# Kernel optimization log

Hardware: AMD Instinct MI355X
Metric: run time of the kernel (lower is better)

Reference implementation:

```python
import jax, jax.numpy as jnp
import numpy as np

D_HIDDEN = 1024
N_HEAD = 16
D_HEAD = D_HIDDEN // N_HEAD  # 64
B, F = 4, 2048


def setup_inputs() -> dict:
    key = jax.random.key(0)
    ks = jax.random.split(key, 10)
    std = 0.02
    inp = {
        "q": jax.random.normal(ks[0], (B, F, D_HIDDEN), jnp.float32),
        "k": jax.random.normal(ks[1], (B, F, D_HIDDEN), jnp.float32),
        "v": jax.random.normal(ks[2], (B, F, D_HIDDEN), jnp.float32),
        # additive mask: 1 = masked position (scaled by -1e9 inside); all-zero = no masking
        "attention_mask": jnp.zeros((B, F, F), jnp.float32),
        # Dense layer params (Keras Dense: y = x @ W + b)
        "qw_w": jax.random.truncated_normal(ks[3], -2, 2, (D_HIDDEN, D_HIDDEN), jnp.float32) * std,
        "qw_b": jnp.zeros((D_HIDDEN,), jnp.float32),
        "kw_w": jax.random.truncated_normal(ks[4], -2, 2, (D_HIDDEN, D_HIDDEN), jnp.float32) * std,
        "kw_b": jnp.zeros((D_HIDDEN,), jnp.float32),
        "vw_w": jax.random.truncated_normal(ks[5], -2, 2, (D_HIDDEN, D_HIDDEN), jnp.float32) * std,
        "vw_b": jnp.zeros((D_HIDDEN,), jnp.float32),
        # output projection kernel (n_head, d_head, d_hidden)
        "out_kernel": jax.random.truncated_normal(ks[6], -2, 2, (N_HEAD, D_HEAD, D_HIDDEN), jnp.float32) * std,
    }
    return inp


def reference(q, k, v, attention_mask, qw_w, qw_b, kw_w, kw_b, vw_w, vw_b, out_kernel):
    b, f, _ = q.shape
    # linear projections
    qh = q @ qw_w + qw_b
    kh = k @ kw_w + kw_b
    vh = v @ vw_w + vw_b
    # split heads: [B, F, H, D] -> [B, H, F, D]
    def split(x):
        return x.reshape(b, -1, N_HEAD, D_HEAD).transpose(0, 2, 1, 3)
    qh, kh, vh = split(qh), split(kh), split(vh)
    # scaled dot-product attention with additive mask (1 -> -1e9)
    scores = jnp.einsum('BNFD,BNfD->BNFf', qh, kh) / jnp.sqrt(jnp.asarray(D_HEAD, qh.dtype))
    scores = scores + attention_mask[:, None, :, :] * jnp.asarray(-1e9, scores.dtype)
    probs = jax.nn.softmax(scores, axis=-1)
    out = jnp.einsum('BNFf,BNfD->BNFD', probs, vh)
    out = out.transpose(0, 2, 1, 3)  # BNFD -> BFND
    return jnp.einsum('BFND,NDM->BFM', out, out_kernel)
```

## Files before the change

kernel.cpp:

```cpp
#include <hip/hip_runtime.h>


typedef unsigned short u16;
typedef __attribute__((ext_vector_type(8))) short short8;
typedef __attribute__((ext_vector_type(4))) float f32x4;
typedef __attribute__((ext_vector_type(16))) float f32x16;

#define SC2 0.18033688011112042f
#define MSC -1.4426950408889634e9f
#define THR 8.0f

__device__ __forceinline__ u16 f2bf(float x) {
  unsigned int u = __float_as_uint(x);
  u += 0x7FFFu + ((u >> 16) & 1u);
  return (u16)(u >> 16);
}

__device__ __forceinline__ void gload16(const void* g, void* l) {
  __builtin_amdgcn_global_load_lds(
      (const __attribute__((address_space(1))) void*)g,
      (__attribute__((address_space(3))) void*)l, 16, 0, 0);
}

__device__ __forceinline__ uint4 pack8(const u16* t) {
  uint4 o;
  o.x = (unsigned)t[0] | ((unsigned)t[1] << 16);
  o.y = (unsigned)t[2] | ((unsigned)t[3] << 16);
  o.z = (unsigned)t[4] | ((unsigned)t[5] << 16);
  o.w = (unsigned)t[6] | ((unsigned)t[7] << 16);
  return o;
}

__device__ __forceinline__ unsigned cvtpk(float lo, float hi) {
  unsigned r;
  asm("v_cvt_pk_bf16_f32 %0, %1, %2" : "=v"(r) : "v"(lo), "v"(hi));
  return r;
}

__global__ __launch_bounds__(256) void cvt3(const float* __restrict__ q,
                                            const float* __restrict__ k,
                                            const float* __restrict__ v,
                                            u16* __restrict__ dq,
                                            u16* __restrict__ dk,
                                            u16* __restrict__ dv) {
  const float* s;
  u16* d;
  switch (blockIdx.y) {
    case 0: s = q; d = dq; break;
    case 1: s = k; d = dk; break;
    default: s = v; d = dv; break;
  }
  int i = blockIdx.x * 256 + threadIdx.x;
  const float4* sp = (const float4*)s;
  float4 a = sp[2 * i], b = sp[2 * i + 1];
  uint4 o;
  o.x = (unsigned)f2bf(a.x) | ((unsigned)f2bf(a.y) << 16);
  o.y = (unsigned)f2bf(a.z) | ((unsigned)f2bf(a.w) << 16);
  o.z = (unsigned)f2bf(b.x) | ((unsigned)f2bf(b.y) << 16);
  o.w = (unsigned)f2bf(b.z) | ((unsigned)f2bf(b.w) << 16);
  ((uint4*)d)[i] = o;
}

__global__ __launch_bounds__(256) void masksum(const float* __restrict__ mask,
                                               unsigned char* __restrict__ msum) {
  int t = blockIdx.x * 256 + threadIdx.x;
  int row = t & 2047;
  int kt = (t >> 11) & 31;
  int b = t >> 16;
  const float4* p =
      (const float4*)(mask + ((size_t)(b * 2048 + row)) * 2048 + kt * 64);
  unsigned acc = 0;
#pragma unroll
  for (int i = 0; i < 16; i++) {
    float4 f = p[i];
    acc |= __float_as_uint(f.x) | __float_as_uint(f.y) |
           __float_as_uint(f.z) | __float_as_uint(f.w);
  }
  msum[t] = acc ? 1 : 0;
}

__global__ __launch_bounds__(256) void wtrans(
    const float* __restrict__ w0, const float* __restrict__ w1,
    const float* __restrict__ w2, const float* __restrict__ w3,
    u16* __restrict__ o0, u16* __restrict__ o1,
    u16* __restrict__ o2, u16* __restrict__ o3) {
  const float* W; u16* O;
  switch (blockIdx.z) {
    case 0: W = w0; O = o0; break;
    case 1: W = w1; O = o1; break;
    case 2: W = w2; O = o2; break;
    default: W = w3; O = o3; break;
  }
  __shared__ u16 T[64][72];
  const int t = threadIdx.x, r = t >> 2, seg = t & 3;
  const int k0 = blockIdx.y * 64, n0 = blockIdx.x * 64;
  const float* src = W + (size_t)(k0 + r) * 1024 + n0 + seg * 16;
#pragma unroll
  for (int jj = 0; jj < 4; jj++) {
    float4 f = ((const float4*)src)[jj];
    T[r][seg * 16 + jj * 4 + 0] = f2bf(f.x);
    T[r][seg * 16 + jj * 4 + 1] = f2bf(f.y);
    T[r][seg * 16 + jj * 4 + 2] = f2bf(f.z);
    T[r][seg * 16 + jj * 4 + 3] = f2bf(f.w);
  }
  __syncthreads();
  u16 tmp[16];
#pragma unroll
  for (int j = 0; j < 16; j++) tmp[j] = T[seg * 16 + j][r];
  u16* dst = O + (size_t)(n0 + r) * 1024 + k0 + seg * 16;
  ((uint4*)dst)[0] = pack8(tmp);
  ((uint4*)dst)[1] = pack8(tmp + 8);
}

__global__ __launch_bounds__(256) void gemm_proj3(
    const u16* __restrict__ Aq, const u16* __restrict__ Ak,
    const u16* __restrict__ Av, const u16* __restrict__ Wq,
    const u16* __restrict__ Wk, const u16* __restrict__ Wv,
    const float* __restrict__ bq, const float* __restrict__ bk,
    const float* __restrict__ bv, u16* __restrict__ oq,
    u16* __restrict__ ok, u16* __restrict__ ovT) {
  constexpr int K = 1024, N = 1024;
  __shared__ u16 sbuf[128 * 136];
  u16* lsA = sbuf;
  u16* lsB = sbuf + 128 * 32;
  const int z = blockIdx.z;
  const u16* A  = (z == 0) ? Aq : (z == 1) ? Ak : Av;
  const u16* Bt = (z == 0) ? Wq : (z == 1) ? Wk : Wv;
  const float* bias = (z == 0) ? bq : (z == 1) ? bk : bv;

  const int tid = threadIdx.x;
  const int w = tid >> 6, lane = tid & 63;
  const int l15 = lane & 15, lg = lane >> 4;
  const int m0 = blockIdx.y << 7, n0 = blockIdx.x << 7;
  const int wr = w >> 1, wc = w & 1;

  f32x4 acc[4][4];
#pragma unroll
  for (int i = 0; i < 4; i++)
#pragma unroll
    for (int j = 0; j < 4; j++) acc[i][j] = f32x4{0.f, 0.f, 0.f, 0.f};

  const u16* As = A + (size_t)(m0 + w * 32 + (lane >> 2)) * K + (lane & 3) * 8;
  const u16* Bs = Bt + (size_t)(n0 + w * 32 + (lane >> 2)) * K + (lane & 3) * 8;
  u16* lA = &lsA[(w * 32) * 32];
  u16* lB = &lsB[(w * 32) * 32];

  for (int k0 = 0; k0 < K; k0 += 32) {
    gload16(As + k0, lA);
    gload16(As + 16 * K + k0, lA + 16 * 32);
    gload16(Bs + k0, lB);
    gload16(Bs + 16 * K + k0, lB + 16 * 32);
    __syncthreads();
    short8 af[4], bfv[4];
#pragma unroll
    for (int mi = 0; mi < 4; mi++)
      af[mi] = *(const short8*)&lsA[(wr * 64 + mi * 16 + l15) * 32 + lg * 8];
#pragma unroll
    for (int nj = 0; nj < 4; nj++)
      bfv[nj] = *(const short8*)&lsB[(wc * 64 + nj * 16 + l15) * 32 + lg * 8];
#pragma unroll
    for (int mi = 0; mi < 4; mi++)
#pragma unroll
      for (int nj = 0; nj < 4; nj++)
        acc[mi][nj] = __builtin_amdgcn_mfma_f32_16x16x32_bf16(af[mi], bfv[nj],
                                                              acc[mi][nj], 0, 0, 0);
    __syncthreads();
  }

  const int crow = m0 + wr * 64 + lg * 4;
  const int ccol = n0 + wc * 64 + l15;
  if (z < 2) {
    u16* C = (z == 0) ? oq : ok;
    const float scl = (z == 0) ? SC2 : 1.0f;
#pragma unroll
    for (int nj = 0; nj < 4; nj++) {
      float bv = bias[ccol + nj * 16];
#pragma unroll
      for (int mi = 0; mi < 4; mi++)
#pragma unroll
        for (int r = 0; r < 4; r++)
          C[(size_t)(crow + mi * 16 + r) * N + ccol + nj * 16] =
              f2bf((acc[mi][nj][r] + bv) * scl);
    }
  } else {
    const int rl = wr * 64 + lg * 4;
    const int cl = wc * 64 + l15;
#pragma unroll
    for (int nj = 0; nj < 4; nj++) {
      float bv = bias[ccol + nj * 16];
#pragma unroll
      for (int mi = 0; mi < 4; mi++)
#pragma unroll
        for (int r = 0; r < 4; r++)
          sbuf[(rl + mi * 16 + r) * 136 + cl + nj * 16] =
              f2bf(acc[mi][nj][r] + bv);
    }
    __syncthreads();
    const int drow = tid >> 1, seg = tid & 1;
    const int b = m0 >> 11;
    const int f0 = (m0 & 2047) + seg * 64;
    u16* dst = ovT + (size_t)(b * 1024 + n0 + drow) * 2048 + f0;
#pragma unroll
    for (int c = 0; c < 8; c++) {
      u16 tmp[8];
#pragma unroll
      for (int j = 0; j < 8; j++)
        tmp[j] = sbuf[(seg * 64 + c * 8 + j) * 136 + drow];
      ((uint4*)dst)[c] = pack8(tmp);
    }
  }
}

__global__ __launch_bounds__(256) void gemm_out(
    const u16* __restrict__ A, const u16* __restrict__ Bt,
    float* __restrict__ C) {
  constexpr int K = 1024, N = 1024;
  __shared__ u16 lsA[128 * 32];
  __shared__ u16 lsB[128 * 32];
  const int tid = threadIdx.x;
  const int w = tid >> 6, lane = tid & 63;
  const int l15 = lane & 15, lg = lane >> 4;
  const int m0 = blockIdx.y << 7, n0 = blockIdx.x << 7;
  const int wr = w >> 1, wc = w & 1;

  f32x4 acc[4][4];
#pragma unroll
  for (int i = 0; i < 4; i++)
#pragma unroll
    for (int j = 0; j < 4; j++) acc[i][j] = f32x4{0.f, 0.f, 0.f, 0.f};

  const u16* As = A + (size_t)(m0 + w * 32 + (lane >> 2)) * K + (lane & 3) * 8;
  const u16* Bs = Bt + (size_t)(n0 + w * 32 + (lane >> 2)) * K + (lane & 3) * 8;
  u16* lA = &lsA[(w * 32) * 32];
  u16* lB = &lsB[(w * 32) * 32];

  for (int k0 = 0; k0 < K; k0 += 32) {
    gload16(As + k0, lA);
    gload16(As + 16 * K + k0, lA + 16 * 32);
    gload16(Bs + k0, lB);
    gload16(Bs + 16 * K + k0, lB + 16 * 32);
    __syncthreads();
    short8 af[4], bfv[4];
#pragma unroll
    for (int mi = 0; mi < 4; mi++)
      af[mi] = *(const short8*)&lsA[(wr * 64 + mi * 16 + l15) * 32 + lg * 8];
#pragma unroll
    for (int nj = 0; nj < 4; nj++)
      bfv[nj] = *(const short8*)&lsB[(wc * 64 + nj * 16 + l15) * 32 + lg * 8];
#pragma unroll
    for (int mi = 0; mi < 4; mi++)
#pragma unroll
      for (int nj = 0; nj < 4; nj++)
        acc[mi][nj] = __builtin_amdgcn_mfma_f32_16x16x32_bf16(af[mi], bfv[nj],
                                                              acc[mi][nj], 0, 0, 0);
    __syncthreads();
  }

  const int crow = m0 + wr * 64 + lg * 4;
  const int ccol = n0 + wc * 64 + l15;
#pragma unroll
  for (int nj = 0; nj < 4; nj++)
#pragma unroll
    for (int mi = 0; mi < 4; mi++)
#pragma unroll
      for (int r = 0; r < 4; r++)
        C[(size_t)(crow + mi * 16 + r) * N + ccol + nj * 16] = acc[mi][nj][r];
}

__global__ __launch_bounds__(512, 4) void attn_fwd(
    const u16* __restrict__ qh, const u16* __restrict__ kh,
    const u16* __restrict__ vhT, const float* __restrict__ mask,
    const unsigned char* __restrict__ msum, u16* __restrict__ aout) {
  __shared__ u16 Kls[2][64][72];
  __shared__ u16 Vls[2][64][72];

  const int tid = threadIdx.x;
  const int w = tid >> 6, lane = tid & 63;
  const int l31 = lane & 31, hi = lane >> 5;
  const int blk = ((blockIdx.x & 7) << 6) | (blockIdx.x >> 3);
  const int qt = blk & 7, bh = blk >> 3, h = bh & 15, b = bh >> 4;
  const int frow = qt * 256 + w * 32;
  const size_t qrow0 = (size_t)b * 2048 + frow;

  short8 qf[4];
#pragma unroll
  for (int ds = 0; ds < 4; ds++)
    qf[ds] = *(const short8*)&qh[(qrow0 + l31) * 1024 + h * 64 + ds * 16 + hi * 8];

  f32x16 zf;
#pragma unroll
  for (int i = 0; i < 16; i++) zf[i] = 0.f;

  f32x16 oacc[2];
#pragma unroll
  for (int i = 0; i < 16; i++) { oacc[0][i] = 0.f; oacc[1][i] = 0.f; }
  float m_run = 0.f, l_run = 0.f;

  const int sr = tid >> 3, seg = tid & 7;
  const u16* Ksrc = kh + ((size_t)b * 2048 + sr) * 1024 + h * 64 + seg * 8;
  const u16* Vsrc = vhT + ((size_t)bh * 64 + sr) * 2048 + seg * 8;
  const unsigned char* msrow = msum + (size_t)b * 65536 + frow + l31;

  uint4 ka0, va0;
  unsigned char mb, mbn;
  {
    uint4 x0 = *(const uint4*)Ksrc;
    uint4 y0 = *(const uint4*)Vsrc;
    *(uint4*)&Kls[0][sr][seg * 8] = x0;
    *(uint4*)&Vls[0][sr][seg * 8] = y0;
    ka0 = *(const uint4*)(Ksrc + 64 * 1024);
    va0 = *(const uint4*)(Vsrc + 64);
    mb = msrow[0];
    mbn = msrow[2048];
  }
  __syncthreads();

  for (int kt = 0; kt < 32; kt++) {
    const int cur = kt & 1;
    const int k0 = kt * 64;
    const int mflag = __any((int)mb);
    mb = mbn;

    if (kt < 31) {
      *(uint4*)&Kls[cur ^ 1][sr][seg * 8] = ka0;
      *(uint4*)&Vls[cur ^ 1][sr][seg * 8] = va0;
    }
    if (kt < 30) {
      ka0 = *(const uint4*)(Ksrc + (size_t)(kt + 2) * 64 * 1024);
      va0 = *(const uint4*)(Vsrc + (kt + 2) * 64);
      mbn = msrow[(size_t)(kt + 2) * 2048];
    }

    f32x16 sacc[2];
#pragma unroll
    for (int kb = 0; kb < 2; kb++) {
      short8 kf[4];
#pragma unroll
      for (int ds = 0; ds < 4; ds++)
        kf[ds] = *(const short8*)&Kls[cur][kb * 32 + l31][ds * 16 + hi * 8];
      __builtin_amdgcn_s_setprio(1);
      sacc[kb] = __builtin_amdgcn_mfma_f32_32x32x16_bf16(kf[0], qf[0], zf, 0, 0, 0);
#pragma unroll
      for (int ds = 1; ds < 4; ds++)
        sacc[kb] = __builtin_amdgcn_mfma_f32_32x32x16_bf16(kf[ds], qf[ds],
                                                           sacc[kb], 0, 0, 0);
      __builtin_amdgcn_s_setprio(0);
    }

    if (mflag) {
      const size_t mrow = ((size_t)b * 2048 + frow + l31) * 2048 + (size_t)k0;
#pragma unroll
      for (int kb = 0; kb < 2; kb++)
#pragma unroll
        for (int r = 0; r < 16; r++) {
          float mv = mask[mrow + kb * 32 + (r & 3) + 8 * (r >> 2) + 4 * hi];
          sacc[kb][r] = fmaf(mv, MSC, sacc[kb][r]);
        }
      float mx[16];
#pragma unroll
      for (int r = 0; r < 16; r++) mx[r] = fmaxf(sacc[0][r], sacc[1][r]);
#pragma unroll
      for (int s = 8; s >= 1; s >>= 1)
#pragma unroll
        for (int r = 0; r < s; r++) mx[r] = fmaxf(mx[r], mx[r + s]);
      float tm = mx[0];
      tm = fmaxf(tm, __shfl_xor(tm, 32, 64));
      if (!__all(tm <= m_run + THR)) {
        float mnew = fmaxf(m_run, tm);
        float al = exp2f(m_run - mnew);
        m_run = mnew;
        l_run *= al;
#pragma unroll
        for (int r = 0; r < 16; r++) {
          float alr = __shfl(al, (r & 3) + 8 * (r >> 2) + 4 * hi, 64);
          oacc[0][r] *= alr;
          oacc[1][r] *= alr;
        }
      }
    }

    float rsp = 0.f, rsq = 0.f;
    unsigned pw[16];
    if (m_run == 0.f) {
#pragma unroll
      for (int kb = 0; kb < 2; kb++)
#pragma unroll
        for (int jp = 0; jp < 2; jp++) {
          float e[8];
#pragma unroll
          for (int t = 0; t < 8; t++)
            e[t] = exp2f(sacc[kb][8 * jp + t]);
          rsp += (e[0] + e[1]) + (e[2] + e[3]);
          rsq += (e[4] + e[5]) + (e[6] + e[7]);
          unsigned ye0 = cvtpk(e[0], e[1]);
          unsigned ye1 = cvtpk(e[2], e[3]);
          unsigned xo0 = cvtpk(e[4], e[5]);
          unsigned xo1 = cvtpk(e[6], e[7]);
          asm volatile("v_permlane32_swap_b32 %0, %1" : "+v"(ye0), "+v"(xo0));
          asm volatile("v_permlane32_swap_b32 %0, %1" : "+v"(ye1), "+v"(xo1));
          const int kk = kb * 2 + jp;
          pw[kk * 4 + 0] = ye0;
          pw[kk * 4 + 1] = ye1;
          pw[kk * 4 + 2] = xo0;
          pw[kk * 4 + 3] = xo1;
        }
    } else {
      const float mm = m_run;
#pragma unroll
      for (int kb = 0; kb < 2; kb++)
#pragma unroll
        for (int jp = 0; jp < 2; jp++) {
          float e[8];
#pragma unroll
          for (int t = 0; t < 8; t++)
            e[t] = exp2f(sacc[kb][8 * jp + t] - mm);
          rsp += (e[0] + e[1]) + (e[2] + e[3]);
          rsq += (e[4] + e[5]) + (e[6] + e[7]);
          unsigned ye0 = cvtpk(e[0], e[1]);
          unsigned ye1 = cvtpk(e[2], e[3]);
          unsigned xo0 = cvtpk(e[4], e[5]);
          unsigned xo1 = cvtpk(e[6], e[7]);
          asm volatile("v_permlane32_swap_b32 %0, %1" : "+v"(ye0), "+v"(xo0));
          asm volatile("v_permlane32_swap_b32 %0, %1" : "+v"(ye1), "+v"(xo1));
          const int kk = kb * 2 + jp;
          pw[kk * 4 + 0] = ye0;
          pw[kk * 4 + 1] = ye1;
          pw[kk * 4 + 2] = xo0;
          pw[kk * 4 + 3] = xo1;
        }
    }
    float rs = rsp + rsq;
    rs += __shfl_xor(rs, 32, 64);
    l_run += rs;

#pragma unroll
    for (int dn = 0; dn < 2; dn++) {
      short8 vf[4];
#pragma unroll
      for (int kk = 0; kk < 4; kk++)
        vf[kk] = *(const short8*)&Vls[cur][dn * 32 + l31][kk * 16 + hi * 8];
      __builtin_amdgcn_s_setprio(1);
#pragma unroll
      for (int kk = 0; kk < 4; kk++) {
        uint4 t4 = {pw[kk * 4 + 0], pw[kk * 4 + 1], pw[kk * 4 + 2], pw[kk * 4 + 3]};
        oacc[dn] = __builtin_amdgcn_mfma_f32_32x32x16_bf16(
            *(short8*)&t4, vf[kk], oacc[dn], 0, 0, 0);
      }
      __builtin_amdgcn_s_setprio(0);
    }

    __syncthreads();
  }

  float inv = 1.0f / l_run;
#pragma unroll
  for (int r = 0; r < 16; r++) {
    const int qr = (r & 3) + 8 * (r >> 2) + 4 * hi;
    float invr = __shfl(inv, qr, 64);
    aout[(qrow0 + qr) * 1024 + h * 64 + l31] = f2bf(oacc[0][r] * invr);
    aout[(qrow0 + qr) * 1024 + h * 64 + 32 + l31] = f2bf(oacc[1][r] * invr);
  }
}

extern "C" void kernel_launch(void* const* d_in, const int* in_sizes, int n_in,
                              void* d_out, int out_size, void* d_ws, size_t ws_size,
                              hipStream_t stream) {
  (void)in_sizes; (void)n_in; (void)out_size; (void)ws_size;
  const float* q    = (const float*)d_in[0];
  const float* k    = (const float*)d_in[1];
  const float* v    = (const float*)d_in[2];
  const float* mask = (const float*)d_in[3];
  const float* qw_w = (const float*)d_in[4];
  const float* qw_b = (const float*)d_in[5];
  const float* kw_w = (const float*)d_in[6];
  const float* kw_b = (const float*)d_in[7];
  const float* vw_w = (const float*)d_in[8];
  const float* vw_b = (const float*)d_in[9];
  const float* wo   = (const float*)d_in[10];

  u16* qbf = (u16*)d_ws;
  u16* kbf = qbf + 8192 * 1024;
  u16* vbf = kbf + 8192 * 1024;
  u16* vhT = vbf + 8192 * 1024;
  u16* qwT = vhT + 8192 * 1024;
  u16* kwT = qwT + 1024 * 1024;
  u16* vwT = kwT + 1024 * 1024;
  u16* woT = vwT + 1024 * 1024;
  u16* attn_o = kbf;
  unsigned char* msumb = (unsigned char*)(woT + 1024 * 1024);
  u16* qh = (u16*)d_out;
  u16* kh = qh + 8192 * 1024;

  cvt3<<<dim3(4096, 3), 256, 0, stream>>>(q, k, v, qbf, kbf, vbf);
  wtrans<<<dim3(16, 16, 4), 256, 0, stream>>>(qw_w, kw_w, vw_w, wo,
                                              qwT, kwT, vwT, woT);
  gemm_proj3<<<dim3(8, 64, 3), 256, 0, stream>>>(qbf, kbf, vbf, qwT, kwT, vwT,
                                                 qw_b, kw_b, vw_b, qh, kh, vhT);
  masksum<<<1024, 256, 0, stream>>>(mask, msumb);
  attn_fwd<<<512, 512, 0, stream>>>(qh, kh, vhT, mask, msumb, attn_o);
  gemm_out<<<dim3(8, 64), 256, 0, stream>>>(attn_o, woT, (float*)d_out);
}
```

Baseline: 268.4 us.

## Fuse fp32-to-bf16 input conversion into projection GEMM A-tile loads

Removes the separate cvt3 kernel and has gemm_proj3 read fp32 q/k/v directly, converting to bf16 in registers with v_cvt_pk_bf16_f32 and storing to LDS, with a one-step register prefetch of the next A tile. This avoids writing and re-reading three bf16 copies of the activations and one kernel launch. In exchange the A operand is now loaded through registers instead of direct global-to-LDS loads, so each projection block reads twice the bytes for A and re-converts it for each of the 8 N-tiles. Workspace layout is reshuffled to match.

Result: slower. 278.7 us (+3.8%).

```diff
diff --git a/kernel.cpp b/kernel.cpp
--- a/kernel.cpp
+++ b/kernel.cpp
@@ -35,30 +35,6 @@
   unsigned r;
   asm("v_cvt_pk_bf16_f32 %0, %1, %2" : "=v"(r) : "v"(lo), "v"(hi));
   return r;
-}
-
-__global__ __launch_bounds__(256) void cvt3(const float* __restrict__ q,
-                                            const float* __restrict__ k,
-                                            const float* __restrict__ v,
-                                            u16* __restrict__ dq,
-                                            u16* __restrict__ dk,
-                                            u16* __restrict__ dv) {
-  const float* s;
-  u16* d;
-  switch (blockIdx.y) {
-    case 0: s = q; d = dq; break;
-    case 1: s = k; d = dk; break;
-    default: s = v; d = dv; break;
-  }
-  int i = blockIdx.x * 256 + threadIdx.x;
-  const float4* sp = (const float4*)s;
-  float4 a = sp[2 * i], b = sp[2 * i + 1];
-  uint4 o;
-  o.x = (unsigned)f2bf(a.x) | ((unsigned)f2bf(a.y) << 16);
-  o.y = (unsigned)f2bf(a.z) | ((unsigned)f2bf(a.w) << 16);
-  o.z = (unsigned)f2bf(b.x) | ((unsigned)f2bf(b.y) << 16);
-  o.w = (unsigned)f2bf(b.z) | ((unsigned)f2bf(b.w) << 16);
-  ((uint4*)d)[i] = o;
 }
 
 __global__ __launch_bounds__(256) void masksum(const float* __restrict__ mask,
@@ -113,8 +89,8 @@
 }
 
 __global__ __launch_bounds__(256) void gemm_proj3(
-    const u16* __restrict__ Aq, const u16* __restrict__ Ak,
-    const u16* __restrict__ Av, const u16* __restrict__ Wq,
+    const float* __restrict__ Aq, const float* __restrict__ Ak,
+    const float* __restrict__ Av, const u16* __restrict__ Wq,
     const u16* __restrict__ Wk, const u16* __restrict__ Wv,
     const float* __restrict__ bq, const float* __restrict__ bk,
     const float* __restrict__ bv, u16* __restrict__ oq,
@@ -124,7 +100,7 @@
   u16* lsA = sbuf;
   u16* lsB = sbuf + 128 * 32;
   const int z = blockIdx.z;
-  const u16* A  = (z == 0) ? Aq : (z == 1) ? Ak : Av;
+  const float* A = (z == 0) ? Aq : (z == 1) ? Ak : Av;
   const u16* Bt = (z == 0) ? Wq : (z == 1) ? Wk : Wv;
   const float* bias = (z == 0) ? bq : (z == 1) ? bk : bv;
 
@@ -140,16 +116,32 @@
 #pragma unroll
     for (int j = 0; j < 4; j++) acc[i][j] = f32x4{0.f, 0.f, 0.f, 0.f};
 
-  const u16* As = A + (size_t)(m0 + w * 32 + (lane >> 2)) * K + (lane & 3) * 8;
+  const float* As = A + (size_t)(m0 + w * 32 + (lane >> 2)) * K + (lane & 3) * 8;
   const u16* Bs = Bt + (size_t)(n0 + w * 32 + (lane >> 2)) * K + (lane & 3) * 8;
-  u16* lA = &lsA[(w * 32) * 32];
   u16* lB = &lsB[(w * 32) * 32];
+  u16* lAw = &lsA[(w * 32 + (lane >> 2)) * 32 + (lane & 3) * 8];
+
+  float4 a0 = *(const float4*)(As);
+  float4 a1 = *(const float4*)(As + 4);
+  float4 a2 = *(const float4*)(As + 16 * K);
+  float4 a3 = *(const float4*)(As + 16 * K + 4);
 
   for (int k0 = 0; k0 < K; k0 += 32) {
-    gload16(As + k0, lA);
-    gload16(As + 16 * K + k0, lA + 16 * 32);
     gload16(Bs + k0, lB);
     gload16(Bs + 16 * K + k0, lB + 16 * 32);
+    uint4 pa, pb;
+    pa.x = cvtpk(a0.x, a0.y); pa.y = cvtpk(a0.z, a0.w);
+    pa.z = cvtpk(a1.x, a1.y); pa.w = cvtpk(a1.z, a1.w);
+    pb.x = cvtpk(a2.x, a2.y); pb.y = cvtpk(a2.z, a2.w);
+    pb.z = cvtpk(a3.x, a3.y); pb.w = cvtpk(a3.z, a3.w);
+    *(uint4*)lAw = pa;
+    *(uint4*)(lAw + 16 * 32) = pb;
+    if (k0 + 32 < K) {
+      a0 = *(const float4*)(As + k0 + 32);
+      a1 = *(const float4*)(As + k0 + 36);
+      a2 = *(const float4*)(As + 16 * K + k0 + 32);
+      a3 = *(const float4*)(As + 16 * K + k0 + 36);
+    }
     __syncthreads();
     short8 af[4], bfv[4];
 #pragma unroll
@@ -478,23 +470,19 @@
   const float* vw_b = (const float*)d_in[9];
   const float* wo   = (const float*)d_in[10];
 
-  u16* qbf = (u16*)d_ws;
-  u16* kbf = qbf + 8192 * 1024;
-  u16* vbf = kbf + 8192 * 1024;
-  u16* vhT = vbf + 8192 * 1024;
-  u16* qwT = vhT + 8192 * 1024;
+  u16* vhT = (u16*)d_ws;
+  u16* qwT = vhT + 4096 * 2048;
   u16* kwT = qwT + 1024 * 1024;
   u16* vwT = kwT + 1024 * 1024;
   u16* woT = vwT + 1024 * 1024;
-  u16* attn_o = kbf;
-  unsigned char* msumb = (unsigned char*)(woT + 1024 * 1024);
+  u16* attn_o = woT + 1024 * 1024;
+  unsigned char* msumb = (unsigned char*)(attn_o + 8192 * 1024);
   u16* qh = (u16*)d_out;
   u16* kh = qh + 8192 * 1024;
 
-  cvt3<<<dim3(4096, 3), 256, 0, stream>>>(q, k, v, qbf, kbf, vbf);
   wtrans<<<dim3(16, 16, 4), 256, 0, stream>>>(qw_w, kw_w, vw_w, wo,
                                               qwT, kwT, vwT, woT);
-  gemm_proj3<<<dim3(8, 64, 3), 256, 0, stream>>>(qbf, kbf, vbf, qwT, kwT, vwT,
+  gemm_proj3<<<dim3(8, 64, 3), 256, 0, stream>>>(q, k, v, qwT, kwT, vwT,
                                                  qw_b, kw_b, vw_b, qh, kh, vhT);
   masksum<<<1024, 256, 0, stream>>>(mask, msumb);
   attn_fwd<<<512, 512, 0, stream>>>(qh, kh, vhT, mask, msumb, attn_o);
```
